# Kernel tuning notes

Hardware: AMD Instinct MI355X
Metric: run time of the kernel (lower is better)

## Reference

```python
import jax, jax.numpy as jnp
import numpy as np

N = 50000   # nodes
E = 800000  # edges (avg degree 16)
IN, HID, OUT = 128, 128, 64


def setup_inputs() -> dict:
    key = jax.random.key(0)
    ks = jax.random.split(key, 8)
    x = jax.random.normal(ks[0], (N, IN), dtype=jnp.float32)
    edge_index = jax.random.randint(ks[1], (2, E), 0, N, dtype=jnp.int32)
    s = 0.05
    W1 = jax.random.normal(ks[2], (IN, HID), dtype=jnp.float32) * s
    b1 = jnp.zeros((HID,), dtype=jnp.float32)
    W2 = jax.random.normal(ks[3], (HID, HID), dtype=jnp.float32) * s
    b2 = jnp.zeros((HID,), dtype=jnp.float32)
    W3 = jax.random.normal(ks[4], (HID, OUT), dtype=jnp.float32) * s
    b3 = jnp.zeros((OUT,), dtype=jnp.float32)
    return {"x": x, "edge_index": edge_index, "W1": W1, "b1": b1,
            "W2": W2, "b2": b2, "W3": W3, "b3": b3}


def _gcn_norm(edge_index, n):
    # PyG GCNConv default: add self-loops, symmetric normalization D^-1/2 A D^-1/2
    loop = jnp.arange(n, dtype=edge_index.dtype)
    src = jnp.concatenate([edge_index[0], loop])  # [E+N]
    dst = jnp.concatenate([edge_index[1], loop])  # [E+N]
    deg = jax.ops.segment_sum(jnp.ones_like(dst, dtype=jnp.float32), dst,
                              num_segments=n)  # degree of destination (col)
    dinv = jax.lax.rsqrt(deg)  # deg >= 1 due to self-loops
    norm = dinv[src] * dinv[dst]  # [E+N]
    return src, dst, norm


def _gcn_conv(x, src, dst, norm, W, b, n):
    h = x @ W                      # [N, F_out]  (transform first, fewer flops)
    msg = h[src] * norm[:, None]   # gather + scale  [E+N, F_out]
    agg = jax.ops.segment_sum(msg, dst, num_segments=n)
    return agg + b


def reference(x, edge_index, W1, b1, W2, b2, W3, b3):
    n = x.shape[0]
    src, dst, norm = _gcn_norm(edge_index, n)
    h = jax.nn.relu(_gcn_conv(x, src, dst, norm, W1, b1, n))
    h = jax.nn.relu(_gcn_conv(h, src, dst, norm, W2, b2, n))
    # dropout p=0.0 / eval mode -> identity
    out = jax.nn.relu(h @ W3 + b3)
    return out
```

## Files before the change

kernel.cpp:

```cpp
#include <hip/hip_runtime.h>
#include <hip/hip_fp16.h>
#include <cstddef>
#include <type_traits>


typedef _Float16 half8 __attribute__((ext_vector_type(8)));
typedef float f32x4 __attribute__((ext_vector_type(4)));

constexpr int CAP = 4608;

__global__ __launch_bounds__(256) void prep(const float* __restrict__ W1,
                                            const float* __restrict__ W2,
                                            const float* __restrict__ W3,
                                            __half* __restrict__ w1t,
                                            __half* __restrict__ w2t,
                                            __half* __restrict__ w3t,
                                            int* __restrict__ gcount, int nb) {
    int b = blockIdx.x;
    if (b == 0 && threadIdx.x < nb) gcount[threadIdx.x] = 0;
    const float* W;
    __half* Wt;
    int ncol, i;
    if (b < 64) { W = W1; Wt = w1t; ncol = 128; i = b * 256 + threadIdx.x; }
    else if (b < 128) { W = W2; Wt = w2t; ncol = 128; i = (b - 64) * 256 + threadIdx.x; }
    else { W = W3; Wt = w3t; ncol = 64; i = (b - 128) * 256 + threadIdx.x; }
    if (i < 128 * ncol) {
        int k = i / ncol, c = i - k * ncol;
        Wt[c * 128 + k] = __float2half(W[i]);
    }
}

__global__ __launch_bounds__(1024) void bucket_p1(const int* __restrict__ src,
                                                  const int* __restrict__ dst,
                                                  int* __restrict__ gcount,
                                                  int2* __restrict__ gbucket,
                                                  int nb, int e) {
    __shared__ int lcnt[256];
    __shared__ int lbase[256];
    int t = threadIdx.x;
    if (t < nb) lcnt[t] = 0;
    __syncthreads();

    int base = blockIdx.x * 8192 + t * 8;
    int d[8], s[8], pb[8], pp[8];
    if (base + 8 <= e) {
        *(int4*)&d[0] = *(const int4*)&dst[base];
        *(int4*)&d[4] = *(const int4*)&dst[base + 4];
        *(int4*)&s[0] = *(const int4*)&src[base];
        *(int4*)&s[4] = *(const int4*)&src[base + 4];
    } else {
#pragma unroll
        for (int u = 0; u < 8; ++u) {
            d[u] = (base + u < e) ? dst[base + u] : -1;
            s[u] = (base + u < e) ? src[base + u] : 0;
        }
    }
#pragma unroll
    for (int u = 0; u < 8; ++u) {
        if (d[u] >= 0) {
            pb[u] = d[u] >> 8;
            pp[u] = atomicAdd(&lcnt[pb[u]], 1);
        }
    }
    __syncthreads();
    if (t < nb) lbase[t] = lcnt[t] ? atomicAdd(&gcount[t], lcnt[t]) : 0;
    __syncthreads();
#pragma unroll
    for (int u = 0; u < 8; ++u) {
        if (d[u] >= 0) {
            int p = lbase[pb[u]] + pp[u];
            if (p < CAP) gbucket[(size_t)pb[u] * CAP + p] = make_int2(d[u], s[u]);
        }
    }
}

__device__ __forceinline__ void gemm_tile_xf32(const float* __restrict__ A,
                                               const __half* __restrict__ Wt,
                                               __half* __restrict__ C, int M,
                                               int tile, int t) {
    constexpr int NC = 4;
    const int w = t >> 6, l = t & 63;
    const int lr = l & 15, kg = l >> 4;
    const int rh = w >> 1, ch = w & 1;
    const int r0 = tile * 64 + rh * 32;

    half8 wf[NC][4];
#pragma unroll
    for (int c = 0; c < NC; ++c)
#pragma unroll
        for (int ks = 0; ks < 4; ++ks)
            wf[c][ks] = *(const half8*)&Wt[(size_t)((ch * NC + c) * 16 + lr) * 128 +
                                           ks * 32 + kg * 8];

    f32x4 acc[2][NC];
#pragma unroll
    for (int rt = 0; rt < 2; ++rt)
#pragma unroll
        for (int c = 0; c < NC; ++c) acc[rt][c] = (f32x4){0.f, 0.f, 0.f, 0.f};

    const int row0 = r0 + lr, row1 = r0 + 16 + lr;
    const bool ok0 = row0 < M, ok1 = row1 < M;
#pragma unroll
    for (int ks = 0; ks < 4; ++ks) {
        half8 af0 = (half8)(_Float16)0, af1 = (half8)(_Float16)0;
        if (ok0) {
            float4 p = *(const float4*)&A[(size_t)row0 * 128 + ks * 32 + kg * 8];
            float4 q = *(const float4*)&A[(size_t)row0 * 128 + ks * 32 + kg * 8 + 4];
            af0[0] = (_Float16)p.x; af0[1] = (_Float16)p.y;
            af0[2] = (_Float16)p.z; af0[3] = (_Float16)p.w;
            af0[4] = (_Float16)q.x; af0[5] = (_Float16)q.y;
            af0[6] = (_Float16)q.z; af0[7] = (_Float16)q.w;
        }
        if (ok1) {
            float4 p = *(const float4*)&A[(size_t)row1 * 128 + ks * 32 + kg * 8];
            float4 q = *(const float4*)&A[(size_t)row1 * 128 + ks * 32 + kg * 8 + 4];
            af1[0] = (_Float16)p.x; af1[1] = (_Float16)p.y;
            af1[2] = (_Float16)p.z; af1[3] = (_Float16)p.w;
            af1[4] = (_Float16)q.x; af1[5] = (_Float16)q.y;
            af1[6] = (_Float16)q.z; af1[7] = (_Float16)q.w;
        }
#pragma unroll
        for (int c = 0; c < NC; ++c) {
            acc[0][c] = __builtin_amdgcn_mfma_f32_16x16x32_f16(wf[c][ks], af0, acc[0][c], 0, 0, 0);
            acc[1][c] = __builtin_amdgcn_mfma_f32_16x16x32_f16(wf[c][ks], af1, acc[1][c], 0, 0, 0);
        }
    }

#pragma unroll
    for (int rt = 0; rt < 2; ++rt) {
        int row = r0 + rt * 16 + lr;
        if (row < M) {
#pragma unroll
            for (int c = 0; c < NC; ++c) {
                int col = (ch * NC + c) * 16 + kg * 4;
                __half2 p0 = __floats2half2_rn(acc[rt][c][0], acc[rt][c][1]);
                __half2 p1 = __floats2half2_rn(acc[rt][c][2], acc[rt][c][3]);
                *(int2*)&C[(size_t)row * 128 + col] = make_int2(*(int*)&p0, *(int*)&p1);
            }
        }
    }
}

__global__ __launch_bounds__(256) void build_and_g1(const int* __restrict__ gcount,
                                                    const int2* __restrict__ gbucket,
                                                    int* __restrict__ offs,
                                                    float* __restrict__ dinv,
                                                    int* __restrict__ eidx,
                                                    const float* __restrict__ x,
                                                    const __half* __restrict__ w1t,
                                                    __half* __restrict__ g1buf,
                                                    int n, int nb) {
    __shared__ int srcS[CAP];
    __shared__ int sc[256];
    __shared__ int cur[256];
    const int bid = blockIdx.x, t = threadIdx.x;

    if (bid >= nb) {
        gemm_tile_xf32(x, w1t, g1buf, n, bid - nb, t);
        return;
    }

    int node0 = bid << 8;
    int own = (t < nb) ? gcount[t] : 0;
    sc[t] = own;
    __syncthreads();
    for (int d = 1; d < 256; d <<= 1) {
        int u = (t >= d) ? sc[t - d] : 0;
        __syncthreads();
        sc[t] += u;
        __syncthreads();
    }
    cur[t] = sc[t] - own;
    if (bid == 0 && t == 0) offs[n] = sc[255];
    __syncthreads();
    int gb = cur[bid];
    int cnt = min(gcount[bid], CAP);
    __syncthreads();

    cur[t] = 0;
    __syncthreads();
    const int2* gbp = gbucket + (size_t)bid * CAP;
    for (int i = t; i < cnt; i += 256) {
        int2 pr = gbp[i];
        atomicAdd(&cur[pr.x - node0], 1);
    }
    __syncthreads();
    own = cur[t];
    sc[t] = own;
    __syncthreads();
    for (int d = 1; d < 256; d <<= 1) {
        int u = (t >= d) ? sc[t - d] : 0;
        __syncthreads();
        sc[t] += u;
        __syncthreads();
    }
    int excl = sc[t] - own;
    int node = node0 + t;
    if (node < n) {
        offs[node] = gb + excl;
        dinv[node] = rsqrtf((float)(own + 1));
    }
    cur[t] = excl;
    __syncthreads();
    for (int i = t; i < cnt; i += 256) {
        int2 pr = gbp[i];
        int pos = atomicAdd(&cur[pr.x - node0], 1);
        srcS[pos] = pr.y;
    }
    __syncthreads();
    for (int i = t; i < cnt; i += 256) eidx[gb + i] = srcS[i];
}

template <int N2, bool EPI, typename OT>
__global__ __launch_bounds__(256) void agg_gemm(const __half* __restrict__ g,
                                                const float* __restrict__ dinv,
                                                const int* __restrict__ offs,
                                                const int* __restrict__ eidx,
                                                const float* __restrict__ biasA,
                                                const __half* __restrict__ Wt,
                                                const float* __restrict__ biasG,
                                                OT* __restrict__ C, int n) {
    __shared__ alignas(16) char hs[16 * 256];
    const int t = threadIdx.x;
    const int node0 = blockIdx.x * 16;

    {
        int row = t >> 4;
        int lane = t & 15;
        int node = node0 + row;
        int bo = (lane * 16) ^ ((row & 7) << 4);
        if (node < n) {
            const int4* h4 = (const int4*)g;
            float dv = dinv[node];
            int4 sp = h4[(size_t)node * 16 + lane];
            float nm = dv * dv;
            float a0, a1, a2, a3, a4, a5, a6, a7;
            {
                float2 f0 = __half22float2(*(__half2*)&sp.x);
                float2 f1 = __half22float2(*(__half2*)&sp.y);
                float2 f2 = __half22float2(*(__half2*)&sp.z);
                float2 f3 = __half22float2(*(__half2*)&sp.w);
                a0 = f0.x * nm; a1 = f0.y * nm; a2 = f1.x * nm; a3 = f1.y * nm;
                a4 = f2.x * nm; a5 = f2.y * nm; a6 = f3.x * nm; a7 = f3.y * nm;
            }
            int beg = offs[node], end = offs[node + 1];
            int j = beg;
            for (; j + 8 <= end; j += 8) {
                int s[8];
                float wg[8];
                int4 hv[8];
#pragma unroll
                for (int u = 0; u < 8; ++u) s[u] = eidx[j + u];
#pragma unroll
                for (int u = 0; u < 8; ++u) {
                    wg[u] = dinv[s[u]];
                    hv[u] = h4[(size_t)s[u] * 16 + lane];
                }
#pragma unroll
                for (int u = 0; u < 8; ++u) {
                    float wu = wg[u] * dv;
                    float2 g0 = __half22float2(*(__half2*)&hv[u].x);
                    float2 g1 = __half22float2(*(__half2*)&hv[u].y);
                    float2 g2 = __half22float2(*(__half2*)&hv[u].z);
                    float2 g3 = __half22float2(*(__half2*)&hv[u].w);
                    a0 = fmaf(g0.x, wu, a0); a1 = fmaf(g0.y, wu, a1);
                    a2 = fmaf(g1.x, wu, a2); a3 = fmaf(g1.y, wu, a3);
                    a4 = fmaf(g2.x, wu, a4); a5 = fmaf(g2.y, wu, a5);
                    a6 = fmaf(g3.x, wu, a6); a7 = fmaf(g3.y, wu, a7);
                }
            }
            if (j < end) {
                int s[8];
                float wg[8];
                int4 hv[8];
#pragma unroll
                for (int u = 0; u < 8; ++u) {
                    int idx = j + u;
                    s[u] = eidx[idx < end ? idx : end - 1];
                }
#pragma unroll
                for (int u = 0; u < 8; ++u) {
                    wg[u] = (j + u < end) ? dinv[s[u]] : 0.f;
                    hv[u] = h4[(size_t)s[u] * 16 + lane];
                }
#pragma unroll
                for (int u = 0; u < 8; ++u) {
                    float wu = wg[u] * dv;
                    float2 g0 = __half22float2(*(__half2*)&hv[u].x);
                    float2 g1 = __half22float2(*(__half2*)&hv[u].y);
                    float2 g2 = __half22float2(*(__half2*)&hv[u].z);
                    float2 g3 = __half22float2(*(__half2*)&hv[u].w);
                    a0 = fmaf(g0.x, wu, a0); a1 = fmaf(g0.y, wu, a1);
                    a2 = fmaf(g1.x, wu, a2); a3 = fmaf(g1.y, wu, a3);
                    a4 = fmaf(g2.x, wu, a4); a5 = fmaf(g2.y, wu, a5);
                    a6 = fmaf(g3.x, wu, a6); a7 = fmaf(g3.y, wu, a7);
                }
            }
            float4 b0 = *(const float4*)&biasA[lane * 8];
            float4 b1 = *(const float4*)&biasA[lane * 8 + 4];
            a0 = fmaxf(a0 + b0.x, 0.f); a1 = fmaxf(a1 + b0.y, 0.f);
            a2 = fmaxf(a2 + b0.z, 0.f); a3 = fmaxf(a3 + b0.w, 0.f);
            a4 = fmaxf(a4 + b1.x, 0.f); a5 = fmaxf(a5 + b1.y, 0.f);
            a6 = fmaxf(a6 + b1.z, 0.f); a7 = fmaxf(a7 + b1.w, 0.f);
            __half2 o0 = __floats2half2_rn(a0, a1);
            __half2 o1 = __floats2half2_rn(a2, a3);
            __half2 o2 = __floats2half2_rn(a4, a5);
            __half2 o3 = __floats2half2_rn(a6, a7);
            *(int4*)&hs[row * 256 + bo] =
                make_int4(*(int*)&o0, *(int*)&o1, *(int*)&o2, *(int*)&o3);
        } else {
            *(int4*)&hs[row * 256 + bo] = make_int4(0, 0, 0, 0);
        }
    }
    __syncthreads();

    constexpr int NW = N2 / 4;
    constexpr int NC = NW / 16;
    const int w = t >> 6, l = t & 63;
    const int lr = l & 15, kg = l >> 4;

    half8 wf[NC][4];
#pragma unroll
    for (int c = 0; c < NC; ++c)
#pragma unroll
        for (int ks = 0; ks < 4; ++ks)
            wf[c][ks] = *(const half8*)&Wt[(size_t)(w * NW + c * 16 + lr) * 128 +
                                           ks * 32 + kg * 8];

    half8 af[4];
#pragma unroll
    for (int ks = 0; ks < 4; ++ks) {
        int bo = (ks * 64 + kg * 16) ^ ((lr & 7) << 4);
        af[ks] = *(const half8*)&hs[lr * 256 + bo];
    }

    f32x4 acc[NC];
#pragma unroll
    for (int c = 0; c < NC; ++c) acc[c] = (f32x4){0.f, 0.f, 0.f, 0.f};
#pragma unroll
    for (int ks = 0; ks < 4; ++ks)
#pragma unroll
        for (int c = 0; c < NC; ++c)
            acc[c] = __builtin_amdgcn_mfma_f32_16x16x32_f16(wf[c][ks], af[ks], acc[c], 0, 0, 0);

    int row = node0 + lr;
    if (row < n) {
#pragma unroll
        for (int c = 0; c < NC; ++c) {
            int col = w * NW + c * 16 + kg * 4;
            float v0 = acc[c][0], v1 = acc[c][1], v2 = acc[c][2], v3 = acc[c][3];
            if constexpr (EPI) {
                float4 bv = *(const float4*)&biasG[col];
                v0 = fmaxf(v0 + bv.x, 0.f);
                v1 = fmaxf(v1 + bv.y, 0.f);
                v2 = fmaxf(v2 + bv.z, 0.f);
                v3 = fmaxf(v3 + bv.w, 0.f);
            }
            if constexpr (std::is_same_v<OT, float>) {
                *(float4*)&C[(size_t)row * N2 + col] = make_float4(v0, v1, v2, v3);
            } else {
                __half2 p0 = __floats2half2_rn(v0, v1);
                __half2 p1 = __floats2half2_rn(v2, v3);
                *(int2*)&C[(size_t)row * N2 + col] = make_int2(*(int*)&p0, *(int*)&p1);
            }
        }
    }
}

extern "C" void kernel_launch(void* const* d_in, const int* in_sizes, int n_in,
                              void* d_out, int out_size, void* d_ws, size_t ws_size,
                              hipStream_t stream) {
    const float* x  = (const float*)d_in[0];
    const int* ei   = (const int*)d_in[1];
    const float* W1 = (const float*)d_in[2];
    const float* b1 = (const float*)d_in[3];
    const float* W2 = (const float*)d_in[4];
    const float* b2 = (const float*)d_in[5];
    const float* W3 = (const float*)d_in[6];
    const float* b3 = (const float*)d_in[7];
    float* out = (float*)d_out;

    const int N = in_sizes[0] / 128;
    const int E = in_sizes[1] / 2;
    const int* esrc = ei;
    const int* edst = ei + E;
    const int nb = (N + 255) >> 8;

    char* w = (char*)d_ws;
    size_t off = 0;
    auto alloc = [&](size_t bytes) {
        void* p = w + off;
        off = (off + bytes + 255) & ~(size_t)255;
        return p;
    };
    int*    gcount  = (int*)alloc((size_t)nb * 4);
    int2*   gbucket = (int2*)alloc((size_t)nb * CAP * 8);
    int*    offs    = (int*)alloc((size_t)(N + 1) * 4);
    float*  dinv    = (float*)alloc((size_t)N * 4);
    int*    eidx    = (int*)alloc((size_t)E * 4);
    __half* w1t     = (__half*)alloc(128 * 128 * 2);
    __half* w2t     = (__half*)alloc(128 * 128 * 2);
    __half* w3t     = (__half*)alloc(64 * 128 * 2);
    __half* g1buf   = (__half*)alloc((size_t)N * 128 * 2);
    __half* g2buf   = (__half*)alloc((size_t)N * 128 * 2);
    (void)ws_size;

    const int gemm_blocks = (N + 63) / 64;
    const int agg_blocks = (N + 15) / 16;

    prep<<<160, 256, 0, stream>>>(W1, W2, W3, w1t, w2t, w3t, gcount, nb);
    bucket_p1<<<(E + 8191) / 8192, 1024, 0, stream>>>(esrc, edst, gcount, gbucket, nb, E);
    build_and_g1<<<nb + gemm_blocks, 256, 0, stream>>>(gcount, gbucket, offs, dinv,
                                                       eidx, x, w1t, g1buf, N, nb);
    agg_gemm<128, false, __half><<<agg_blocks, 256, 0, stream>>>(
        g1buf, dinv, offs, eidx, b1, w2t, nullptr, g2buf, N);
    agg_gemm<64, true, float><<<agg_blocks, 256, 0, stream>>>(
        g2buf, dinv, offs, eidx, b2, w3t, b3, out, N);
}
```

Measured before the change: 116.1 us.

## Pre-scale features by dinv, drop per-edge dinv gathers, cooperative edge index loads

Result: slower. 119.7 us (+3.1%).

```diff
diff --git a/kernel.cpp b/kernel.cpp
--- a/kernel.cpp
+++ b/kernel.cpp
@@ -74,8 +74,25 @@
     }
 }
 
+__global__ __launch_bounds__(256) void hist_dinv(const int* __restrict__ gcount,
+                                                 const int2* __restrict__ gbucket,
+                                                 float* __restrict__ dinv, int n) {
+    __shared__ int cur[256];
+    int b = blockIdx.x, t = threadIdx.x;
+    int node0 = b << 8;
+    cur[t] = 0;
+    __syncthreads();
+    int cnt = min(gcount[b], CAP);
+    const int2* gbp = gbucket + (size_t)b * CAP;
+    for (int i = t; i < cnt; i += 256) atomicAdd(&cur[gbp[i].x - node0], 1);
+    __syncthreads();
+    int node = node0 + t;
+    if (node < n) dinv[node] = rsqrtf((float)(cur[t] + 1));
+}
+
 __device__ __forceinline__ void gemm_tile_xf32(const float* __restrict__ A,
                                                const __half* __restrict__ Wt,
+                                               const float* __restrict__ dinv,
                                                __half* __restrict__ C, int M,
                                                int tile, int t) {
     constexpr int NC = 4;
@@ -130,11 +147,12 @@
     for (int rt = 0; rt < 2; ++rt) {
         int row = r0 + rt * 16 + lr;
         if (row < M) {
+            float dvr = dinv[row];
 #pragma unroll
             for (int c = 0; c < NC; ++c) {
                 int col = (ch * NC + c) * 16 + kg * 4;
-                __half2 p0 = __floats2half2_rn(acc[rt][c][0], acc[rt][c][1]);
-                __half2 p1 = __floats2half2_rn(acc[rt][c][2], acc[rt][c][3]);
+                __half2 p0 = __floats2half2_rn(acc[rt][c][0] * dvr, acc[rt][c][1] * dvr);
+                __half2 p1 = __floats2half2_rn(acc[rt][c][2] * dvr, acc[rt][c][3] * dvr);
                 *(int2*)&C[(size_t)row * 128 + col] = make_int2(*(int*)&p0, *(int*)&p1);
             }
         }
@@ -144,7 +162,7 @@
 __global__ __launch_bounds__(256) void build_and_g1(const int* __restrict__ gcount,
                                                     const int2* __restrict__ gbucket,
                                                     int* __restrict__ offs,
-                                                    float* __restrict__ dinv,
+                                                    const float* __restrict__ dinv,
                                                     int* __restrict__ eidx,
                                                     const float* __restrict__ x,
                                                     const __half* __restrict__ w1t,
@@ -156,7 +174,7 @@
     const int bid = blockIdx.x, t = threadIdx.x;
 
     if (bid >= nb) {
-        gemm_tile_xf32(x, w1t, g1buf, n, bid - nb, t);
+        gemm_tile_xf32(x, w1t, dinv, g1buf, n, bid - nb, t);
         return;
     }
 
@@ -196,10 +214,7 @@
     }
     int excl = sc[t] - own;
     int node = node0 + t;
-    if (node < n) {
-        offs[node] = gb + excl;
-        dinv[node] = rsqrtf((float)(own + 1));
-    }
+    if (node < n) offs[node] = gb + excl;
     cur[t] = excl;
     __syncthreads();
     for (int i = t; i < cnt; i += 256) {
@@ -211,7 +226,7 @@
     for (int i = t; i < cnt; i += 256) eidx[gb + i] = srcS[i];
 }
 
-template <int N2, bool EPI, typename OT>
+template <int N2, bool EPI, typename OT, bool OUT_PRE>
 __global__ __launch_bounds__(256) void agg_gemm(const __half* __restrict__ g,
                                                 const float* __restrict__ dinv,
                                                 const int* __restrict__ offs,
@@ -227,75 +242,59 @@
     {
         int row = t >> 4;
         int lane = t & 15;
+        int wl = t & 63;
+        int gbase = wl & 48;
         int node = node0 + row;
         int bo = (lane * 16) ^ ((row & 7) << 4);
         if (node < n) {
             const int4* h4 = (const int4*)g;
             float dv = dinv[node];
             int4 sp = h4[(size_t)node * 16 + lane];
-            float nm = dv * dv;
             float a0, a1, a2, a3, a4, a5, a6, a7;
             {
                 float2 f0 = __half22float2(*(__half2*)&sp.x);
                 float2 f1 = __half22float2(*(__half2*)&sp.y);
                 float2 f2 = __half22float2(*(__half2*)&sp.z);
                 float2 f3 = __half22float2(*(__half2*)&sp.w);
-                a0 = f0.x * nm; a1 = f0.y * nm; a2 = f1.x * nm; a3 = f1.y * nm;
-                a4 = f2.x * nm; a5 = f2.y * nm; a6 = f3.x * nm; a7 = f3.y * nm;
+                a0 = f0.x; a1 = f0.y; a2 = f1.x; a3 = f1.y;
+                a4 = f2.x; a5 = f2.y; a6 = f3.x; a7 = f3.y;
             }
             int beg = offs[node], end = offs[node + 1];
-            int j = beg;
-            for (; j + 8 <= end; j += 8) {
-                int s[8];
-                float wg[8];
+            int eirg = 0;
+            if (end > beg) {
+                int i0 = beg + (wl & 7);
+                eirg = eidx[i0 < end ? i0 : end - 1];
+            }
+            for (int j = beg; j < end; j += 8) {
+                int nj = j + 8;
+                int eirg_n = eirg;
+                if (nj < end) {
+                    int ni = nj + (wl & 7);
+                    eirg_n = eidx[ni < end ? ni : end - 1];
+                }
                 int4 hv[8];
-#pragma unroll
-                for (int u = 0; u < 8; ++u) s[u] = eidx[j + u];
+                float wgt[8];
 #pragma unroll
                 for (int u = 0; u < 8; ++u) {
-                    wg[u] = dinv[s[u]];
-                    hv[u] = h4[(size_t)s[u] * 16 + lane];
+                    int s = __shfl(eirg, gbase + u, 64);
+                    wgt[u] = (j + u < end) ? 1.f : 0.f;
+                    hv[u] = h4[(size_t)s * 16 + lane];
                 }
 #pragma unroll
                 for (int u = 0; u < 8; ++u) {
-                    float wu = wg[u] * dv;
                     float2 g0 = __half22float2(*(__half2*)&hv[u].x);
                     float2 g1 = __half22float2(*(__half2*)&hv[u].y);
                     float2 g2 = __half22float2(*(__half2*)&hv[u].z);
                     float2 g3 = __half22float2(*(__half2*)&hv[u].w);
-                    a0 = fmaf(g0.x, wu, a0); a1 = fmaf(g0.y, wu, a1);
-                    a2 = fmaf(g1.x, wu, a2); a3 = fmaf(g1.y, wu, a3);
-                    a4 = fmaf(g2.x, wu, a4); a5 = fmaf(g2.y, wu, a5);
-                    a6 = fmaf(g3.x, wu, a6); a7 = fmaf(g3.y, wu, a7);
+                    a0 = fmaf(g0.x, wgt[u], a0); a1 = fmaf(g0.y, wgt[u], a1);
+                    a2 = fmaf(g1.x, wgt[u], a2); a3 = fmaf(g1.y, wgt[u], a3);
+                    a4 = fmaf(g2.x, wgt[u], a4); a5 = fmaf(g2.y, wgt[u], a5);
+                    a6 = fmaf(g3.x, wgt[u], a6); a7 = fmaf(g3.y, wgt[u], a7);
                 }
-            }
-            if (j < end) {
-                int s[8];
-                float wg[8];
-                int4 hv[8];
-#pragma unroll
-                for (int u = 0; u < 8; ++u) {
-                    int idx = j + u;
-                    s[u] = eidx[idx < end ? idx : end - 1];
-                }
-#pragma unroll
-                for (int u = 0; u < 8; ++u) {
-                    wg[u] = (j + u < end) ? dinv[s[u]] : 0.f;
-                    hv[u] = h4[(size_t)s[u] * 16 + lane];
-                }
-#pragma unroll
-                for (int u = 0; u < 8; ++u) {
-                    float wu = wg[u] * dv;
-                    float2 g0 = __half22float2(*(__half2*)&hv[u].x);
-                    float2 g1 = __half22float2(*(__half2*)&hv[u].y);
-                    float2 g2 = __half22float2(*(__half2*)&hv[u].z);
-                    float2 g3 = __half22float2(*(__half2*)&hv[u].w);
-                    a0 = fmaf(g0.x, wu, a0); a1 = fmaf(g0.y, wu, a1);
-                    a2 = fmaf(g1.x, wu, a2); a3 = fmaf(g1.y, wu, a3);
-                    a4 = fmaf(g2.x, wu, a4); a5 = fmaf(g2.y, wu, a5);
-                    a6 = fmaf(g3.x, wu, a6); a7 = fmaf(g3.y, wu, a7);
-                }
-            }
+                eirg = eirg_n;
+            }
+            a0 *= dv; a1 *= dv; a2 *= dv; a3 *= dv;
+            a4 *= dv; a5 *= dv; a6 *= dv; a7 *= dv;
             float4 b0 = *(const float4*)&biasA[lane * 8];
             float4 b1 = *(const float4*)&biasA[lane * 8 + 4];
             a0 = fmaxf(a0 + b0.x, 0.f); a1 = fmaxf(a1 + b0.y, 0.f);
@@ -345,6 +344,7 @@
 
     int row = node0 + lr;
     if (row < n) {
+        float dvr = OUT_PRE ? dinv[row] : 1.f;
 #pragma unroll
         for (int c = 0; c < NC; ++c) {
             int col = w * NW + c * 16 + kg * 4;
@@ -356,6 +356,7 @@
                 v2 = fmaxf(v2 + bv.z, 0.f);
                 v3 = fmaxf(v3 + bv.w, 0.f);
             }
+            if constexpr (OUT_PRE) { v0 *= dvr; v1 *= dvr; v2 *= dvr; v3 *= dvr; }
             if constexpr (std::is_same_v<OT, float>) {
                 *(float4*)&C[(size_t)row * N2 + col] = make_float4(v0, v1, v2, v3);
             } else {
@@ -410,10 +411,11 @@
 
     prep<<<160, 256, 0, stream>>>(W1, W2, W3, w1t, w2t, w3t, gcount, nb);
     bucket_p1<<<(E + 8191) / 8192, 1024, 0, stream>>>(esrc, edst, gcount, gbucket, nb, E);
+    hist_dinv<<<nb, 256, 0, stream>>>(gcount, gbucket, dinv, N);
     build_and_g1<<<nb + gemm_blocks, 256, 0, stream>>>(gcount, gbucket, offs, dinv,
                                                        eidx, x, w1t, g1buf, N, nb);
-    agg_gemm<128, false, __half><<<agg_blocks, 256, 0, stream>>>(
+    agg_gemm<128, false, __half, true><<<agg_blocks, 256, 0, stream>>>(
         g1buf, dinv, offs, eidx, b1, w2t, nullptr, g2buf, N);
-    agg_gemm<64, true, float><<<agg_blocks, 256, 0, stream>>>(
+    agg_gemm<64, true, float, false><<<agg_blocks, 256, 0, stream>>>(
         g2buf, dinv, offs, eidx, b2, w3t, b3, out, N);
 }
```
